# Kernel optimization log

Hardware: AMD Instinct MI355X
Metric: run time of the kernel (lower is better)

Reference implementation:

```python
import jax, jax.numpy as jnp
import numpy as np

B, S, D, N = 4, 2048, 256, 12  # batch, seq_len, hidden_size(=size_per_head), heads


def setup_inputs() -> dict:
    key = jax.random.key(0)
    k1, k2, k3, k4, k5 = jax.random.split(key, 5)
    std = 0.02
    return {
        "input_tensor": jax.random.normal(k1, (B, S, D), dtype=jnp.float32),
        "attention_mask": jnp.ones((B, S, S), dtype=jnp.int32),
        "qk_kernel": jax.random.normal(k2, (D, N, D), dtype=jnp.float32) * std,
        "qk_bias": jnp.zeros((N, D), dtype=jnp.float32),
        "v_kernel": jax.random.normal(k3, (D, N, D), dtype=jnp.float32) * std,
        "v_bias": jnp.zeros((N, D), dtype=jnp.float32),
    }


def reference(input_tensor, attention_mask, qk_kernel, qk_bias, v_kernel, v_bias):
    # Dense3D projections: [B,F,D_in] x [D_in,N,D] -> [B,F,N,D]
    query_key = jnp.einsum('bfc,cnd->bfnd', input_tensor, qk_kernel) + qk_bias
    value = jnp.einsum('bfc,cnd->bfnd', input_tensor, v_kernel) + v_bias
    # scores[b,n,s,f] = sum_d query_key[b,f,n,d] * input_tensor[b,s,d]
    # (original broadcasts input over heads; broadcasting is implicit here)
    scores = jnp.einsum('bfnd,bsd->bnsf', query_key, input_tensor)
    adder = (1.0 - attention_mask.astype(scores.dtype)) * -10000.0  # [B,S,F]
    scores = scores + adder[:, None, :, :]  # broadcast over heads
    probs = jax.nn.softmax(scores, axis=-1)  # softmax over F
    # dropout rate is 0.0 -> identity
    # context [B,S,N,D] then sum over heads -> fuse into one einsum [B,S,D]
    out = jnp.einsum('bnsf,bfnd->bsd', probs, value)
    return out
```

## Files before the change

### kernel.cpp

```cpp
#include <hip/hip_runtime.h>
#include <stdint.h>

#define B_ 4
#define S_ 2048
#define D_ 256
#define NH_ 12
#define M_ (B_*S_)
#define J_ (NH_*D_)
#define LOG2E_ 1.4426950408889634f

typedef __bf16 bf16;
typedef __bf16 bf16x8 __attribute__((ext_vector_type(8)));
typedef __bf16 bf16x4 __attribute__((ext_vector_type(4)));
typedef float  f32x4  __attribute__((ext_vector_type(4)));

#define MFMA16(a,b,c) __builtin_amdgcn_mfma_f32_16x16x32_bf16(a,b,c,0,0,0)

__device__ __forceinline__ void g2lds16(void* l, const void* g) {
  __builtin_amdgcn_global_load_lds(
      (const __attribute__((address_space(1))) unsigned int*)g,
      (__attribute__((address_space(3))) unsigned int*)l, 16, 0, 0);
}

__global__ __launch_bounds__(256) void prep_k(const float* __restrict__ X,
                                              bf16* __restrict__ Xbf,
                                              const float* __restrict__ Wqk,
                                              bf16* __restrict__ Wqkt,
                                              const float* __restrict__ Wv,
                                              bf16* __restrict__ Wvt) {
  int bid = blockIdx.x;
  if (bid < 2048) {
    int i = bid * 256 + threadIdx.x;
    f32x4 v = *(const f32x4*)(X + (size_t)i * 4);
    bf16x4 o;
#pragma unroll
    for (int k = 0; k < 4; ++k) o[k] = (bf16)v[k];
    *(bf16x4*)(Xbf + (size_t)i * 4) = o;
  } else {
    int q = bid - 2048;
    const float* W = (q >= 192) ? Wv : Wqk;
    bf16* Wt       = (q >= 192) ? Wvt : Wqkt;
    q %= 192;
    int c0 = (q / 12) * 16;
    int j  = (q % 12) * 256 + threadIdx.x;
    bf16x8 v0, v1;
#pragma unroll
    for (int i = 0; i < 8; ++i) v0[i] = (bf16)W[(size_t)(c0 + i) * J_ + j];
#pragma unroll
    for (int i = 0; i < 8; ++i) v1[i] = (bf16)W[(size_t)(c0 + 8 + i) * J_ + j];
    *(bf16x8*)(Wt + (size_t)j * D_ + c0)     = v0;
    *(bf16x8*)(Wt + (size_t)j * D_ + c0 + 8) = v1;
  }
}

__device__ __forceinline__ void mask_flags_body(const int* __restrict__ mask,
                                                int* __restrict__ flags, int bx) {
  int ft = bx & 31, st = (bx >> 5) & 31, b = bx >> 10;
  int t = threadIdx.x;
  const int4* mp4 = (const int4*)(mask + (size_t)b * S_ * S_ +
                                  (size_t)(st * 64 + (t >> 2)) * S_ + ft * 64 + (t & 3) * 16);
  bool ok = true;
#pragma unroll
  for (int i = 0; i < 4; ++i) {
    int4 v = mp4[i];
    ok &= (v.x == 1) & (v.y == 1) & (v.z == 1) & (v.w == 1);
  }
  __shared__ int flag;
  if (t == 0) flag = 1;
  __syncthreads();
  if (!ok) flag = 0;
  __syncthreads();
  if (t == 0) flags[bx] = flag;
}

__device__ __forceinline__ void gemm_body(
    const bf16* __restrict__ A, const bf16* __restrict__ Bm,
    const float* __restrict__ bias, bf16* __restrict__ C,
    int Ndim, int bias_mode, float scale, int bid)
{
  __shared__ bf16 As[2][128 * 64];
  __shared__ bf16 Bs[2][128 * 64];
  const int nbn = Ndim >> 7;
  const int bm = bid / nbn, bn = bid % nbn;
  const int t = threadIdx.x, w = t >> 6, l = t & 63;
  const int lane16 = l & 15, quad = l >> 4;
  const int wm = (w & 1) << 6, wn = (w >> 1) << 6;
  const int srow = t >> 3;
  const int gc = (t & 7) ^ (srow & 7);
  const bf16* Ag = A + (size_t)((bm << 7) + srow) * 256 + gc * 8;
  const bf16* Bg = Bm + (size_t)((bn << 7) + srow) * 256 + gc * 8;

  auto stage = [&](int buf, int k0) {
#pragma unroll
    for (int i = 0; i < 4; ++i)
      g2lds16(&As[buf][(size_t)(i * 256 + (w << 6)) * 8], Ag + (size_t)i * 32 * 256 + k0);
#pragma unroll
    for (int i = 0; i < 4; ++i)
      g2lds16(&Bs[buf][(size_t)(i * 256 + (w << 6)) * 8], Bg + (size_t)i * 32 * 256 + k0);
  };

  f32x4 acc[4][4] = {};
  stage(0, 0);
  int cur = 0;
  for (int k0 = 0; k0 < 256; k0 += 64) {
    __syncthreads();
    if (k0 + 64 < 256) stage(cur ^ 1, k0 + 64);
#pragma unroll
    for (int kt = 0; kt < 2; ++kt) {
      bf16x8 af[4], bfr[4];
#pragma unroll
      for (int i = 0; i < 4; ++i)
        af[i] = *(const bf16x8*)(&As[cur][(wm + i * 16 + lane16) * 64 +
                                 (((kt * 4 + quad) ^ (lane16 & 7)) * 8)]);
#pragma unroll
      for (int i = 0; i < 4; ++i)
        bfr[i] = *(const bf16x8*)(&Bs[cur][(wn + i * 16 + lane16) * 64 +
                                  (((kt * 4 + quad) ^ (lane16 & 7)) * 8)]);
#pragma unroll
      for (int i = 0; i < 4; ++i)
#pragma unroll
        for (int jx = 0; jx < 4; ++jx)
          acc[i][jx] = MFMA16(af[i], bfr[jx], acc[i][jx]);
    }
    cur ^= 1;
  }
#pragma unroll
  for (int i = 0; i < 4; ++i)
#pragma unroll
    for (int jx = 0; jx < 4; ++jx) {
      int col = (bn << 7) + wn + jx * 16 + lane16;
#pragma unroll
      for (int r = 0; r < 4; ++r) {
        int row = (bm << 7) + wm + i * 16 + quad * 4 + r;
        float v = (acc[i][jx][r] + (bias_mode ? bias[row] : bias[col])) * scale;
        C[(size_t)row * Ndim + col] = (bf16)v;
      }
    }
}

__global__ __launch_bounds__(256) void gemm_flags(
    const bf16* __restrict__ Xbf, const bf16* __restrict__ Wqkt,
    const float* __restrict__ bqk, bf16* __restrict__ QKw,
    const bf16* __restrict__ Wvt, const float* __restrict__ bv,
    bf16* __restrict__ Vtw,
    const int* __restrict__ mask, int* __restrict__ flags)
{
  int bid = blockIdx.x;
  if (bid < 1536)      gemm_body(Xbf, Wqkt, bqk, QKw, J_, 0, LOG2E_, bid);
  else if (bid < 3072) gemm_body(Wvt, Xbf, bv, Vtw, M_, 1, 1.0f, bid - 1536);
  else                 mask_flags_body(mask, flags, bid - 3072);
}

template<int HS>
__global__ __launch_bounds__(256, 2) void attn_k(
    const bf16* __restrict__ X, const bf16* __restrict__ QK, const bf16* __restrict__ Vt,
    const int* __restrict__ mask, const int* __restrict__ flags,
    bf16* __restrict__ Part, float* __restrict__ Lsum)
{
  __shared__ bf16 Ks[2][32 * 256];
  __shared__ bf16 Vs[2][256 * 32];
  __shared__ bf16 Ps[4][32 * 40];
  const int i  = blockIdx.x;
  const int x  = i & 7, rr = i >> 3;
  const int gh = x + 8 * (rr >> 4);
  const int st = rr & 15;
  const int h  = HS ? (gh >= 48 ? 1 : 0) : 0;
  const int g  = gh - 48 * h;
  const int b  = g / 12, n = g % 12;
  const int f_beg = h * 1024;
  const int f_end = f_beg + (HS ? 1024 : 2048);
  const int t = threadIdx.x, w = t >> 6, l = t & 63;
  const int lane16 = l & 15, quad = l >> 4;
  const int sw = (st << 7) + (w << 5);
  const bf16* Xb = X + (size_t)b * S_ * D_;
  bf16x8 qf[2][8];
#pragma unroll
  for (int ts = 0; ts < 2; ++ts)
#pragma unroll
    for (int kt = 0; kt < 8; ++kt)
      qf[ts][kt] = *(const bf16x8*)(Xb + (size_t)(sw + ts * 16 + lane16) * D_ + kt * 32 + quad * 8);
  const bf16* QKb = QK + (size_t)b * S_ * J_ + n * D_;
  const bf16* Vtb = Vt + (size_t)n * D_ * M_ + (size_t)b * S_;
  const int* flagb = flags + (b * 32 + st * 2 + (w >> 1)) * 32;
  f32x4 oacc[8][4] = {};
  float lsum[2] = {0.f, 0.f};

  auto stage = [&](int buf, int f0) {
#pragma unroll
    for (int ii = 0; ii < 4; ++ii) {
      int frow = ii * 8 + (t >> 5);
      int dc = (t & 31) ^ (frow & 7);
      g2lds16(&Ks[buf][ii * 2048 + (w << 9)], QKb + (size_t)(f0 + frow) * J_ + dc * 8);
    }
#pragma unroll
    for (int ii = 0; ii < 4; ++ii) {
      int drow = ii * 64 + (t >> 2);
      int fc = (t & 3) ^ ((drow >> 1) & 3);
      g2lds16(&Vs[buf][ii * 2048 + (w << 9)], Vtb + (size_t)drow * M_ + f0 + fc * 8);
    }
  };

  stage(0, f_beg);
  int cur = 0;
  for (int f0 = f_beg; f0 < f_end; f0 += 32) {
    __syncthreads();
    if (f0 + 32 < f_end) stage(cur ^ 1, f0 + 32);
    f32x4 sfr[2][2] = {};
    __builtin_amdgcn_s_setprio(1);
#pragma unroll
    for (int kt = 0; kt < 8; ++kt)
#pragma unroll
      for (int ct = 0; ct < 2; ++ct) {
        int fl = ct * 16 + lane16;
        bf16x8 kf = *(const bf16x8*)(&Ks[cur][fl * 256 + (((kt * 4 + quad) ^ (fl & 7)) * 8)]);
        sfr[0][ct] = MFMA16(kf, qf[0][kt], sfr[0][ct]);
        sfr[1][ct] = MFMA16(kf, qf[1][kt], sfr[1][ct]);
      }
    __builtin_amdgcn_s_setprio(0);
    float ex[2][2][4];
    if (flagb[f0 >> 6]) {
#pragma unroll
      for (int ts = 0; ts < 2; ++ts)
#pragma unroll
        for (int ct = 0; ct < 2; ++ct)
#pragma unroll
          for (int r = 0; r < 4; ++r)
            ex[ts][ct][r] = __builtin_amdgcn_exp2f(sfr[ts][ct][r]);
    } else {
#pragma unroll
      for (int ts = 0; ts < 2; ++ts)
#pragma unroll
        for (int ct = 0; ct < 2; ++ct)
#pragma unroll
          for (int r = 0; r < 4; ++r) {
            int s = sw + ts * 16 + lane16, f = f0 + ct * 16 + quad * 4 + r;
            float add = (1.0f - (float)mask[(size_t)b * S_ * S_ + (size_t)s * S_ + f])
                        * (-10000.0f * LOG2E_);
            ex[ts][ct][r] = __builtin_amdgcn_exp2f(sfr[ts][ct][r] + add);
          }
    }
#pragma unroll
    for (int ts = 0; ts < 2; ++ts)
      lsum[ts] += ex[ts][0][0] + ex[ts][0][1] + ex[ts][0][2] + ex[ts][0][3]
                + ex[ts][1][0] + ex[ts][1][1] + ex[ts][1][2] + ex[ts][1][3];
#pragma unroll
    for (int ts = 0; ts < 2; ++ts)
#pragma unroll
      for (int ct = 0; ct < 2; ++ct) {
        int base = (ts * 16 + lane16) * 40 + ct * 16 + quad * 4;
        bf16x4 pv;
        pv[0] = (bf16)ex[ts][ct][0]; pv[1] = (bf16)ex[ts][ct][1];
        pv[2] = (bf16)ex[ts][ct][2]; pv[3] = (bf16)ex[ts][ct][3];
        *(bf16x4*)(&Ps[w][base]) = pv;
      }
    asm volatile("s_waitcnt lgkmcnt(0)\n\ts_barrier" ::: "memory");
    bf16x8 vfr[4];
#pragma unroll
    for (int dtile = 0; dtile < 4; ++dtile) {
      int dl = (w << 6) + dtile * 16 + lane16;
      vfr[dtile] = *(const bf16x8*)(&Vs[cur][dl * 32 + ((quad ^ ((dl >> 1) & 3)) * 8)]);
    }
    __builtin_amdgcn_s_setprio(1);
#pragma unroll
    for (int stile = 0; stile < 8; ++stile) {
      bf16x8 pfr = *(const bf16x8*)(&Ps[stile >> 1][(((stile & 1) << 4) + lane16) * 40 + quad * 8]);
#pragma unroll
      for (int dtile = 0; dtile < 4; ++dtile)
        oacc[stile][dtile] = MFMA16(pfr, vfr[dtile], oacc[stile][dtile]);
    }
    __builtin_amdgcn_s_setprio(0);
    cur ^= 1;
  }
  float tot[2];
#pragma unroll
  for (int ts = 0; ts < 2; ++ts) {
    float rs = lsum[ts];
    rs += __shfl_xor(rs, 16);
    rs += __shfl_xor(rs, 32);
    tot[ts] = rs;
  }
  bf16*  Cb = Part + (size_t)(h * 48 + g) * S_ * D_;
  float* Lb = Lsum + (size_t)(h * 48 + g) * S_;
  if (l < 16) {
#pragma unroll
    for (int ts = 0; ts < 2; ++ts) Lb[sw + ts * 16 + l] = tot[ts];
  }
#pragma unroll
  for (int stile = 0; stile < 8; ++stile)
#pragma unroll
    for (int r = 0; r < 4; ++r) {
      int s = (st << 7) + stile * 16 + quad * 4 + r;
#pragma unroll
      for (int dtile = 0; dtile < 4; ++dtile) {
        int d = (w << 6) + dtile * 16 + lane16;
        Cb[(size_t)s * D_ + d] = (bf16)oacc[stile][dtile][r];
      }
    }
}

template<int HS>
__global__ __launch_bounds__(256) void head_sum(const bf16* __restrict__ Part,
                                                const float* __restrict__ Lsum,
                                                float* __restrict__ out) {
  int i = blockIdx.x * 256 + threadIdx.x;
  int m = i >> 5;
  int dc = (i & 31) * 8;
  int b = m >> 11, s = m & 2047;
  float acc[8] = {};
#pragma unroll
  for (int n = 0; n < NH_; ++n) {
    int g = b * NH_ + n;
    const bf16* p = Part + ((size_t)g * S_ + s) * D_ + dc;
    float lv = Lsum[(size_t)g * S_ + s];
    bf16x8 v0 = *(const bf16x8*)p;
    float a[8];
#pragma unroll
    for (int k = 0; k < 8; ++k) a[k] = (float)v0[k];
    if (HS) {
      lv += Lsum[(size_t)(48 + g) * S_ + s];
      bf16x8 v1 = *(const bf16x8*)(p + (size_t)48 * S_ * D_);
#pragma unroll
      for (int k = 0; k < 8; ++k) a[k] += (float)v1[k];
    }
    float inv = 1.0f / lv;
#pragma unroll
    for (int k = 0; k < 8; ++k) acc[k] += a[k] * inv;
  }
  f32x4 o0, o1;
#pragma unroll
  for (int k = 0; k < 4; ++k) { o0[k] = acc[k]; o1[k] = acc[4 + k]; }
  float* q = out + (size_t)m * D_ + dc;
  *(f32x4*)q = o0;
  *(f32x4*)(q + 4) = o1;
}

extern "C" void kernel_launch(void* const* d_in, const int* in_sizes, int n_in,
                              void* d_out, int out_size, void* d_ws, size_t ws_size,
                              hipStream_t stream) {
  (void)in_sizes; (void)n_in; (void)out_size;
  const float* X    = (const float*)d_in[0];
  const int*   mask = (const int*)d_in[1];
  const float* Wqk  = (const float*)d_in[2];
  const float* bqk  = (const float*)d_in[3];
  const float* Wv   = (const float*)d_in[4];
  const float* bv   = (const float*)d_in[5];
  float* out = (float*)d_out;

  char* p = (char*)d_ws;
  bf16*  Xbf  = (bf16*)p;  p += (size_t)M_ * D_ * 2;
  bf16*  Wqkt = (bf16*)p;  p += (size_t)J_ * D_ * 2;
  bf16*  Wvt  = (bf16*)p;  p += (size_t)J_ * D_ * 2;
  bf16*  QKw  = (bf16*)p;  p += (size_t)M_ * J_ * 2;
  bf16*  Vtw  = (bf16*)p;  p += (size_t)J_ * M_ * 2;
  int*   flags= (int*)p;   p += 4096 * 4;
  float* Lsum = (float*)p; p += (size_t)2 * 48 * S_ * 4;
  bf16*  Part = (bf16*)p;
  size_t need = (size_t)(p - (char*)d_ws) + (size_t)2 * 48 * S_ * D_ * 2;
  int hs = (ws_size >= need) ? 1 : 0;

  prep_k<<<2048 + 384, 256, 0, stream>>>(X, Xbf, Wqk, Wqkt, Wv, Wvt);
  gemm_flags<<<3072 + 4096, 256, 0, stream>>>(Xbf, Wqkt, bqk, QKw, Wvt, bv, Vtw,
                                              mask, flags);
  if (hs) {
    attn_k<1><<<B_ * NH_ * (S_ / 128) * 2, 256, 0, stream>>>(Xbf, QKw, Vtw, mask, flags, Part, Lsum);
    head_sum<1><<<(M_ * D_ / 8) / 256, 256, 0, stream>>>(Part, Lsum, out);
  } else {
    attn_k<0><<<B_ * NH_ * (S_ / 128), 256, 0, stream>>>(Xbf, QKw, Vtw, mask, flags, Part, Lsum);
    head_sum<0><<<(M_ * D_ / 8) / 256, 256, 0, stream>>>(Part, Lsum, out);
  }
}
```

Measured before the change: 396.1 us.

## Use 512-thread attention blocks with 64-wide key tiles split across wave halves

Doubles the attention workgroup to 8 waves and processes 64 keys per iteration. The two wave halves each compute scores for 32 keys, write them into a shared probability tile, then each wave accumulates output for a 32-column slice of D over all 128 queries. Row sums are combined across the two halves through LDS before being written out. Each wave now holds half as many accumulator registers and the loop runs half as many barriers, but LDS use roughly doubles, which may reduce how many blocks fit per CU.

```diff
diff --git a/kernel.cpp b/kernel.cpp
--- a/kernel.cpp
+++ b/kernel.cpp
@@ -152,14 +152,15 @@
 }
 
 template<int HS>
-__global__ __launch_bounds__(256, 2) void attn_k(
+__global__ __launch_bounds__(512, 2) void attn_k(
     const bf16* __restrict__ X, const bf16* __restrict__ QK, const bf16* __restrict__ Vt,
     const int* __restrict__ mask, const int* __restrict__ flags,
     bf16* __restrict__ Part, float* __restrict__ Lsum)
 {
-  __shared__ bf16 Ks[2][32 * 256];
-  __shared__ bf16 Vs[2][256 * 32];
-  __shared__ bf16 Ps[4][32 * 40];
+  __shared__ bf16 Ks[2][64 * 256];
+  __shared__ bf16 Vs[2][256 * 64];
+  __shared__ bf16 Ps[128 * 72];
+  __shared__ float Ls[8][32];
   const int i  = blockIdx.x;
   const int x  = i & 7, rr = i >> 3;
   const int gh = x + 8 * (rr >> 4);
@@ -171,7 +172,9 @@
   const int f_end = f_beg + (HS ? 1024 : 2048);
   const int t = threadIdx.x, w = t >> 6, l = t & 63;
   const int lane16 = l & 15, quad = l >> 4;
-  const int sw = (st << 7) + (w << 5);
+  const int wsg = w & 3;
+  const int wfh = w >> 2;
+  const int sw = (st << 7) + (wsg << 5);
   const bf16* Xb = X + (size_t)b * S_ * D_;
   bf16x8 qf[2][8];
 #pragma unroll
@@ -181,37 +184,37 @@
       qf[ts][kt] = *(const bf16x8*)(Xb + (size_t)(sw + ts * 16 + lane16) * D_ + kt * 32 + quad * 8);
   const bf16* QKb = QK + (size_t)b * S_ * J_ + n * D_;
   const bf16* Vtb = Vt + (size_t)n * D_ * M_ + (size_t)b * S_;
-  const int* flagb = flags + (b * 32 + st * 2 + (w >> 1)) * 32;
-  f32x4 oacc[8][4] = {};
+  const int* flagb = flags + (b * 32 + st * 2 + (wsg >> 1)) * 32;
+  f32x4 oacc[8][2] = {};
   float lsum[2] = {0.f, 0.f};
 
   auto stage = [&](int buf, int f0) {
 #pragma unroll
     for (int ii = 0; ii < 4; ++ii) {
-      int frow = ii * 8 + (t >> 5);
+      int frow = ii * 16 + (t >> 5);
       int dc = (t & 31) ^ (frow & 7);
-      g2lds16(&Ks[buf][ii * 2048 + (w << 9)], QKb + (size_t)(f0 + frow) * J_ + dc * 8);
+      g2lds16(&Ks[buf][ii * 4096 + (w << 9)], QKb + (size_t)(f0 + frow) * J_ + dc * 8);
     }
 #pragma unroll
     for (int ii = 0; ii < 4; ++ii) {
-      int drow = ii * 64 + (t >> 2);
-      int fc = (t & 3) ^ ((drow >> 1) & 3);
-      g2lds16(&Vs[buf][ii * 2048 + (w << 9)], Vtb + (size_t)drow * M_ + f0 + fc * 8);
+      int drow = ii * 64 + (t >> 3);
+      int fc = (t & 7) ^ (drow & 7);
+      g2lds16(&Vs[buf][ii * 4096 + (w << 9)], Vtb + (size_t)drow * M_ + f0 + fc * 8);
     }
   };
 
   stage(0, f_beg);
   int cur = 0;
-  for (int f0 = f_beg; f0 < f_end; f0 += 32) {
+  for (int f0 = f_beg; f0 < f_end; f0 += 64) {
     __syncthreads();
-    if (f0 + 32 < f_end) stage(cur ^ 1, f0 + 32);
+    if (f0 + 64 < f_end) stage(cur ^ 1, f0 + 64);
     f32x4 sfr[2][2] = {};
     __builtin_amdgcn_s_setprio(1);
 #pragma unroll
     for (int kt = 0; kt < 8; ++kt)
 #pragma unroll
       for (int ct = 0; ct < 2; ++ct) {
-        int fl = ct * 16 + lane16;
+        int fl = (wfh << 5) + ct * 16 + lane16;
         bf16x8 kf = *(const bf16x8*)(&Ks[cur][fl * 256 + (((kt * 4 + quad) ^ (fl & 7)) * 8)]);
         sfr[0][ct] = MFMA16(kf, qf[0][kt], sfr[0][ct]);
         sfr[1][ct] = MFMA16(kf, qf[1][kt], sfr[1][ct]);
@@ -233,7 +236,8 @@
         for (int ct = 0; ct < 2; ++ct)
 #pragma unroll
           for (int r = 0; r < 4; ++r) {
-            int s = sw + ts * 16 + lane16, f = f0 + ct * 16 + quad * 4 + r;
+            int s = sw + ts * 16 + lane16;
+            int f = f0 + (wfh << 5) + ct * 16 + quad * 4 + r;
             float add = (1.0f - (float)mask[(size_t)b * S_ * S_ + (size_t)s * S_ + f])
                         * (-10000.0f * LOG2E_);
             ex[ts][ct][r] = __builtin_amdgcn_exp2f(sfr[ts][ct][r] + add);
@@ -247,26 +251,31 @@
     for (int ts = 0; ts < 2; ++ts)
 #pragma unroll
       for (int ct = 0; ct < 2; ++ct) {
-        int base = (ts * 16 + lane16) * 40 + ct * 16 + quad * 4;
+        int base = ((wsg << 5) + ts * 16 + lane16) * 72 + (wfh << 5) + ct * 16 + quad * 4;
         bf16x4 pv;
         pv[0] = (bf16)ex[ts][ct][0]; pv[1] = (bf16)ex[ts][ct][1];
         pv[2] = (bf16)ex[ts][ct][2]; pv[3] = (bf16)ex[ts][ct][3];
-        *(bf16x4*)(&Ps[w][base]) = pv;
+        *(bf16x4*)(&Ps[base]) = pv;
       }
     asm volatile("s_waitcnt lgkmcnt(0)\n\ts_barrier" ::: "memory");
-    bf16x8 vfr[4];
-#pragma unroll
-    for (int dtile = 0; dtile < 4; ++dtile) {
-      int dl = (w << 6) + dtile * 16 + lane16;
-      vfr[dtile] = *(const bf16x8*)(&Vs[cur][dl * 32 + ((quad ^ ((dl >> 1) & 3)) * 8)]);
-    }
+    bf16x8 vfr[2][2];
+#pragma unroll
+    for (int dtile = 0; dtile < 2; ++dtile)
+#pragma unroll
+      for (int kc = 0; kc < 2; ++kc) {
+        int dl = (w << 5) + dtile * 16 + lane16;
+        vfr[dtile][kc] = *(const bf16x8*)(&Vs[cur][dl * 64 + (((kc * 4 + quad) ^ (dl & 7)) * 8)]);
+      }
     __builtin_amdgcn_s_setprio(1);
 #pragma unroll
     for (int stile = 0; stile < 8; ++stile) {
-      bf16x8 pfr = *(const bf16x8*)(&Ps[stile >> 1][(((stile & 1) << 4) + lane16) * 40 + quad * 8]);
-#pragma unroll
-      for (int dtile = 0; dtile < 4; ++dtile)
-        oacc[stile][dtile] = MFMA16(pfr, vfr[dtile], oacc[stile][dtile]);
+      const bf16* prow = &Ps[(stile * 16 + lane16) * 72 + quad * 8];
+      bf16x8 pf0 = *(const bf16x8*)(prow);
+      bf16x8 pf1 = *(const bf16x8*)(prow + 32);
+      oacc[stile][0] = MFMA16(pf0, vfr[0][0], oacc[stile][0]);
+      oacc[stile][0] = MFMA16(pf1, vfr[0][1], oacc[stile][0]);
+      oacc[stile][1] = MFMA16(pf0, vfr[1][0], oacc[stile][1]);
+      oacc[stile][1] = MFMA16(pf1, vfr[1][1], oacc[stile][1]);
     }
     __builtin_amdgcn_s_setprio(0);
     cur ^= 1;
@@ -279,11 +288,17 @@
     rs += __shfl_xor(rs, 32);
     tot[ts] = rs;
   }
+  if (l < 16) {
+#pragma unroll
+    for (int ts = 0; ts < 2; ++ts) Ls[w][ts * 16 + l] = tot[ts];
+  }
+  __syncthreads();
   bf16*  Cb = Part + (size_t)(h * 48 + g) * S_ * D_;
   float* Lb = Lsum + (size_t)(h * 48 + g) * S_;
-  if (l < 16) {
-#pragma unroll
-    for (int ts = 0; ts < 2; ++ts) Lb[sw + ts * 16 + l] = tot[ts];
+  if (w < 4 && l < 16) {
+#pragma unroll
+    for (int ts = 0; ts < 2; ++ts)
+      Lb[(st << 7) + (w << 5) + ts * 16 + l] = Ls[w][ts * 16 + l] + Ls[w + 4][ts * 16 + l];
   }
 #pragma unroll
   for (int stile = 0; stile < 8; ++stile)
@@ -291,8 +306,8 @@
     for (int r = 0; r < 4; ++r) {
       int s = (st << 7) + stile * 16 + quad * 4 + r;
 #pragma unroll
-      for (int dtile = 0; dtile < 4; ++dtile) {
-        int d = (w << 6) + dtile * 16 + lane16;
+      for (int dtile = 0; dtile < 2; ++dtile) {
+        int d = (w << 5) + dtile * 16 + lane16;
         Cb[(size_t)s * D_ + d] = (bf16)oacc[stile][dtile][r];
       }
     }
@@ -362,10 +377,10 @@
   gemm_flags<<<3072 + 4096, 256, 0, stream>>>(Xbf, Wqkt, bqk, QKw, Wvt, bv, Vtw,
                                               mask, flags);
   if (hs) {
-    attn_k<1><<<B_ * NH_ * (S_ / 128) * 2, 256, 0, stream>>>(Xbf, QKw, Vtw, mask, flags, Part, Lsum);
+    attn_k<1><<<B_ * NH_ * (S_ / 128) * 2, 512, 0, stream>>>(Xbf, QKw, Vtw, mask, flags, Part, Lsum);
     head_sum<1><<<(M_ * D_ / 8) / 256, 256, 0, stream>>>(Part, Lsum, out);
   } else {
-    attn_k<0><<<B_ * NH_ * (S_ / 128), 256, 0, stream>>>(Xbf, QKw, Vtw, mask, flags, Part, Lsum);
+    attn_k<0><<<B_ * NH_ * (S_ / 128), 512, 0, stream>>>(Xbf, QKw, Vtw, mask, flags, Part, Lsum);
     head_sum<0><<<(M_ * D_ / 8) / 256, 256, 0, stream>>>(Part, Lsum, out);
   }
 }
```

After: 446.0 us. 1.13x slower.
